# Kernel optimization log

Hardware: AMD Instinct MI355X
Metric: run time of the kernel (lower is better)

Reference implementation:

```python
import jax, jax.numpy as jnp
import numpy as np

D_MODEL = 1024
NUM_HEADS = 16
D_K = D_MODEL // NUM_HEADS
SCALE = float(np.sqrt(D_K))


def setup_inputs() -> dict:
    key = jax.random.key(0)
    ks = jax.random.split(key, 11)
    B, S = 2, 2048
    s = 0.02
    return {
        "query": jax.random.normal(ks[0], (B, S, D_MODEL), dtype=jnp.float32),
        "key_in": jax.random.normal(ks[1], (B, S, D_MODEL), dtype=jnp.float32),
        "value": jax.random.normal(ks[2], (B, S, D_MODEL), dtype=jnp.float32),
        "w_q": jax.random.normal(ks[3], (D_MODEL, D_MODEL), dtype=jnp.float32) * s,
        "b_q": jnp.zeros((D_MODEL,), dtype=jnp.float32),
        "w_k": jax.random.normal(ks[4], (D_MODEL, D_MODEL), dtype=jnp.float32) * s,
        "b_k": jnp.zeros((D_MODEL,), dtype=jnp.float32),
        "w_v": jax.random.normal(ks[5], (D_MODEL, D_MODEL), dtype=jnp.float32) * s,
        "b_v": jnp.zeros((D_MODEL,), dtype=jnp.float32),
        "w_o": jax.random.normal(ks[6], (D_MODEL, D_MODEL), dtype=jnp.float32) * s,
        "b_o": jnp.zeros((D_MODEL,), dtype=jnp.float32),
    }


def _mha(query, key_in, value, w_q, b_q, w_k, b_k, w_v, b_v, w_o, b_o):
    B, S, _ = query.shape
    # linear projections (x @ W + b), split into heads: [B, H, S, Dk]
    def proj(x, w, b):
        y = x @ w + b
        return y.reshape(B, -1, NUM_HEADS, D_K).transpose(0, 2, 1, 3)

    Q = proj(query, w_q, b_q)
    K = proj(key_in, w_k, b_k)
    V = proj(value, w_v, b_v)

    # scores: [B, H, Sq, Sk]
    scores = jnp.einsum("bhqd,bhkd->bhqk", Q, K) / SCALE
    attn = jax.nn.softmax(scores, axis=-1)  # dropout is identity in eval mode
    out = jnp.einsum("bhqk,bhkd->bhqd", attn, V)
    out = out.transpose(0, 2, 1, 3).reshape(B, S, D_MODEL)
    return out @ w_o + b_o


def reference(query, key_in, value, w_q, b_q, w_k, b_k, w_v, b_v, w_o, b_o):
    return _mha(query, key_in, value, w_q, b_q, w_k, b_k, w_v, b_v, w_o, b_o)
```

## Files before the change

### kernel.cpp

```cpp
#include <hip/hip_runtime.h>
#include <cstdint>

#define S_LEN 2048
#define DMODEL 1024
#define NHEADS 16
#define DK 64
#define BATCH 2
#define M_TOT 4096

typedef __attribute__((ext_vector_type(8)))  short  short8;
typedef __attribute__((ext_vector_type(4)))  float  f32x4;
typedef __attribute__((ext_vector_type(16))) float  f32x16;

__device__ __forceinline__ ushort f2bf(float f) {
    union { float f; uint32_t u; } v; v.f = f;
    uint32_t r = (v.u + 0x7fffu + ((v.u >> 16) & 1u)) >> 16;
    return (ushort)r;
}
__device__ __forceinline__ float bf2f(ushort u) {
    union { uint32_t u; float f; } v; v.u = ((uint32_t)u) << 16;
    return v.f;
}

__device__ __forceinline__ void gl_lds16(const void* g, void* l) {
    __builtin_amdgcn_global_load_lds(
        (const __attribute__((address_space(1))) void*)(g),
        (__attribute__((address_space(3))) void*)(l), 16, 0, 0);
}

__global__ __launch_bounds__(256)
void conv3_kernel(const float* __restrict__ a0, const float* __restrict__ a1,
                  const float* __restrict__ a2, ushort* __restrict__ o0,
                  ushort* __restrict__ o1, ushort* __restrict__ o2, int n8)
{
    const float*  in  = blockIdx.z == 0 ? a0 : (blockIdx.z == 1 ? a1 : a2);
    ushort*       out = blockIdx.z == 0 ? o0 : (blockIdx.z == 1 ? o1 : o2);
    int i = blockIdx.x * 256 + threadIdx.x;
    const int stride = gridDim.x * 256;
    for (; i < n8; i += stride) {
        const float4* p = (const float4*)(in + (size_t)i * 8);
        float4 a = p[0], b = p[1];
        ushort r[8];
        r[0]=f2bf(a.x); r[1]=f2bf(a.y); r[2]=f2bf(a.z); r[3]=f2bf(a.w);
        r[4]=f2bf(b.x); r[5]=f2bf(b.y); r[6]=f2bf(b.z); r[7]=f2bf(b.w);
        *(ushort4*)(out + (size_t)i * 8)     = *(ushort4*)&r[0];
        *(ushort4*)(out + (size_t)i * 8 + 4) = *(ushort4*)&r[4];
    }
}

__global__ __launch_bounds__(256)
void wtrans3_kernel(const float* __restrict__ wq, const float* __restrict__ wk,
                    const float* __restrict__ wv, ushort* __restrict__ oq,
                    ushort* __restrict__ ok, ushort* __restrict__ ov)
{
    const float* w  = blockIdx.z == 0 ? wq : (blockIdx.z == 1 ? wk : wv);
    ushort*      hi = blockIdx.z == 0 ? oq : (blockIdx.z == 1 ? ok : ov);

    __shared__ float t[64][65];
    const int n0 = blockIdx.x * 64, k0 = blockIdx.y * 64;
    const int r  = threadIdx.x >> 2;
    const int cb = (threadIdx.x & 3) * 16;

    #pragma unroll
    for (int j = 0; j < 4; ++j) {
        float4 v = *(const float4*)(w + (size_t)(k0 + r) * DMODEL + n0 + cb + j * 4);
        t[r][cb + j*4 + 0] = v.x;
        t[r][cb + j*4 + 1] = v.y;
        t[r][cb + j*4 + 2] = v.z;
        t[r][cb + j*4 + 3] = v.w;
    }
    __syncthreads();

    ushort h8[16];
    #pragma unroll
    for (int j = 0; j < 16; ++j) h8[j] = f2bf(t[cb + j][r]);
    ushort* dsth = hi + (size_t)(n0 + r) * DMODEL + k0 + cb;
    *(ushort4*)(dsth + 0)  = *(ushort4*)&h8[0];
    *(ushort4*)(dsth + 4)  = *(ushort4*)&h8[4];
    *(ushort4*)(dsth + 8)  = *(ushort4*)&h8[8];
    *(ushort4*)(dsth + 12) = *(ushort4*)&h8[12];
}

__global__ __launch_bounds__(256)
void wtrans_o_kernel(const float* __restrict__ w, ushort* __restrict__ hi,
                     ushort* __restrict__ lo)
{
    __shared__ float t[64][65];
    const int n0 = blockIdx.x * 64, k0 = blockIdx.y * 64;
    const int r  = threadIdx.x >> 2;
    const int cb = (threadIdx.x & 3) * 16;

    #pragma unroll
    for (int j = 0; j < 4; ++j) {
        float4 v = *(const float4*)(w + (size_t)(k0 + r) * DMODEL + n0 + cb + j * 4);
        t[r][cb + j*4 + 0] = v.x;
        t[r][cb + j*4 + 1] = v.y;
        t[r][cb + j*4 + 2] = v.z;
        t[r][cb + j*4 + 3] = v.w;
    }
    __syncthreads();

    ushort h8[16], l8[16];
    #pragma unroll
    for (int j = 0; j < 16; ++j) {
        float x = t[cb + j][r];
        ushort h = f2bf(x);
        h8[j] = h;
        l8[j] = f2bf(x - bf2f(h));
    }
    ushort* dsth = hi + (size_t)(n0 + r) * DMODEL + k0 + cb;
    ushort* dstl = lo + (size_t)(n0 + r) * DMODEL + k0 + cb;
    #pragma unroll
    for (int j = 0; j < 4; ++j) {
        *(ushort4*)(dsth + j*4) = *(ushort4*)&h8[j*4];
        *(ushort4*)(dstl + j*4) = *(ushort4*)&l8[j*4];
    }
}

template<int OMODE>
__global__ __launch_bounds__(256)
void gemm_bf16_kernel(const ushort* __restrict__ A, const ushort* __restrict__ Bt,
                      const float* __restrict__ bias, ushort* __restrict__ out,
                      float oscale)
{
    __shared__ __align__(16) ushort lds[2][12288];

    const int t = threadIdx.x, wv = t >> 6, lane = t & 63;
    const int c = lane & 15, g = lane >> 4;
    const int m0 = blockIdx.y * 128, n0 = blockIdx.x * 64;
    const int wr = wv >> 1, wc = wv & 1;
    const int lrow = lane >> 3, lcol = lane & 7;

    f32x4 acc[4][2];
    #pragma unroll
    for (int i = 0; i < 4; ++i)
        #pragma unroll
        for (int j = 0; j < 2; ++j)
            acc[i][j] = (f32x4){0.f, 0.f, 0.f, 0.f};

    auto stage = [&](int buf, int kt) {
        #pragma unroll
        for (int j = 0; j < 6; ++j) {
            const int ci = wv * 6 + j;
            ushort* dst = &lds[buf][ci * 512];
            const ushort* src;
            if (ci < 16) {
                const int row  = ci * 8 + lrow;
                const int colb = (lcol * 16) ^ ((row & 7) << 4);
                src = A + (size_t)(m0 + row) * 1024 + kt * 64 + (colb >> 1);
            } else {
                const int row  = (ci - 16) * 8 + lrow;
                const int colb = (lcol * 16) ^ ((row & 7) << 4);
                src = Bt + (size_t)(n0 + row) * 1024 + kt * 64 + (colb >> 1);
            }
            gl_lds16(src, dst);
        }
    };

    stage(0, 0);
    __syncthreads();

    for (int kt = 0; kt < 16; ++kt) {
        const int cur = kt & 1;
        if (kt < 15) stage(cur ^ 1, kt + 1);

        const char* la = (const char*)&lds[cur][0];
        const char* lb = (const char*)&lds[cur][8192];
        #pragma unroll
        for (int kk = 0; kk < 2; ++kk) {
            short8 af[4], bf[2];
            #pragma unroll
            for (int mf = 0; mf < 4; ++mf) {
                const int row = wr * 64 + mf * 16 + c;
                af[mf] = *(const short8*)(la + row * 128 +
                          ((kk * 64 + g * 16) ^ ((c & 7) << 4)));
            }
            #pragma unroll
            for (int nf = 0; nf < 2; ++nf) {
                const int row = wc * 32 + nf * 16 + c;
                bf[nf] = *(const short8*)(lb + row * 128 +
                          ((kk * 64 + g * 16) ^ ((c & 7) << 4)));
            }
            #pragma unroll
            for (int mf = 0; mf < 4; ++mf)
                #pragma unroll
                for (int nf = 0; nf < 2; ++nf)
                    acc[mf][nf] = __builtin_amdgcn_mfma_f32_16x16x32_bf16(
                        af[mf], bf[nf], acc[mf][nf], 0, 0, 0);
        }
        __syncthreads();
    }

    const int b      = m0 >> 11;
    const int s_base = m0 & 2047;
    #pragma unroll
    for (int nf = 0; nf < 2; ++nf) {
        const int ncol = n0 + wc * 32 + nf * 16 + c;
        const float bv = bias[ncol];
        const int h = ncol >> 6, dk = ncol & 63;
        #pragma unroll
        for (int mf = 0; mf < 4; ++mf) {
            if (OMODE == 1) {
                #pragma unroll
                for (int j = 0; j < 4; ++j) {
                    const int s = s_base + wr * 64 + mf * 16 + g * 4 + j;
                    out[(((size_t)(b * NHEADS + h) * S_LEN + s) * DK) + dk] =
                        f2bf((acc[mf][nf][j] + bv) * oscale);
                }
            } else {
                ushort4 v4;
                v4.x = f2bf((acc[mf][nf][0] + bv) * oscale);
                v4.y = f2bf((acc[mf][nf][1] + bv) * oscale);
                v4.z = f2bf((acc[mf][nf][2] + bv) * oscale);
                v4.w = f2bf((acc[mf][nf][3] + bv) * oscale);
                const int s = s_base + wr * 64 + mf * 16 + g * 4;
                *(ushort4*)&out[((size_t)(b * NHEADS + h) * DK + dk) * S_LEN + s] = v4;
            }
        }
    }
}

__global__ __launch_bounds__(256)
void gemm_split_kernel(const ushort* __restrict__ Ahi, const ushort* __restrict__ Alo,
                       const ushort* __restrict__ Bhi, const ushort* __restrict__ Blo,
                       const float* __restrict__ bias, float* __restrict__ out)
{
    __shared__ __align__(16) ushort lds[24576];

    const int t = threadIdx.x, wv = t >> 6, lane = t & 63;
    const int c = lane & 15, g = lane >> 4;
    const int m0 = blockIdx.y * 128, n0 = blockIdx.x * 64;
    const int wr = wv >> 1, wc = wv & 1;
    const int lrow = lane >> 3, lcol = lane & 7;

    f32x4 acc[4][2];
    #pragma unroll
    for (int i = 0; i < 4; ++i)
        #pragma unroll
        for (int j = 0; j < 2; ++j)
            acc[i][j] = (f32x4){0.f, 0.f, 0.f, 0.f};

    for (int kt = 0; kt < 16; ++kt) {
        if (kt) __syncthreads();
        #pragma unroll
        for (int j = 0; j < 12; ++j) {
            const int ci = wv * 12 + j;
            ushort* dst = &lds[ci * 512];
            const ushort* src;
            int row, colb;
            if (ci < 16) {
                row = ci * 8 + lrow; colb = (lcol*16) ^ ((row&7)<<4);
                src = Ahi + (size_t)(m0+row)*1024 + kt*64 + (colb>>1);
            } else if (ci < 32) {
                row = (ci-16)*8 + lrow; colb = (lcol*16) ^ ((row&7)<<4);
                src = Alo + (size_t)(m0+row)*1024 + kt*64 + (colb>>1);
            } else if (ci < 40) {
                row = (ci-32)*8 + lrow; colb = (lcol*16) ^ ((row&7)<<4);
                src = Bhi + (size_t)(n0+row)*1024 + kt*64 + (colb>>1);
            } else {
                row = (ci-40)*8 + lrow; colb = (lcol*16) ^ ((row&7)<<4);
                src = Blo + (size_t)(n0+row)*1024 + kt*64 + (colb>>1);
            }
            gl_lds16(src, dst);
        }
        __syncthreads();

        const char* lah = (const char*)&lds[0];
        const char* lal = (const char*)&lds[8192];
        const char* lbh = (const char*)&lds[16384];
        const char* lbl = (const char*)&lds[20480];
        #pragma unroll
        for (int kk = 0; kk < 2; ++kk) {
            short8 ah[4], al[4], bh[2], bl[2];
            #pragma unroll
            for (int mf = 0; mf < 4; ++mf) {
                const int row = wr*64 + mf*16 + c;
                const int off = row*128 + ((kk*64 + g*16) ^ ((c&7)<<4));
                ah[mf] = *(const short8*)(lah + off);
                al[mf] = *(const short8*)(lal + off);
            }
            #pragma unroll
            for (int nf = 0; nf < 2; ++nf) {
                const int row = wc*32 + nf*16 + c;
                const int off = row*128 + ((kk*64 + g*16) ^ ((c&7)<<4));
                bh[nf] = *(const short8*)(lbh + off);
                bl[nf] = *(const short8*)(lbl + off);
            }
            #pragma unroll
            for (int mf = 0; mf < 4; ++mf)
                #pragma unroll
                for (int nf = 0; nf < 2; ++nf) {
                    acc[mf][nf] = __builtin_amdgcn_mfma_f32_16x16x32_bf16(ah[mf], bh[nf], acc[mf][nf], 0,0,0);
                    acc[mf][nf] = __builtin_amdgcn_mfma_f32_16x16x32_bf16(ah[mf], bl[nf], acc[mf][nf], 0,0,0);
                    acc[mf][nf] = __builtin_amdgcn_mfma_f32_16x16x32_bf16(al[mf], bh[nf], acc[mf][nf], 0,0,0);
                }
        }
    }

    #pragma unroll
    for (int nf = 0; nf < 2; ++nf) {
        const int ncol = n0 + wc*32 + nf*16 + c;
        const float bv = bias[ncol];
        #pragma unroll
        for (int mf = 0; mf < 4; ++mf)
            #pragma unroll
            for (int j = 0; j < 4; ++j) {
                const int m = m0 + wr*64 + mf*16 + g*4 + j;
                out[(size_t)m * 1024 + ncol] = acc[mf][nf][j] + bv;
            }
    }
}

__global__ __launch_bounds__(256, 2)
void attn_kernel4(const ushort* __restrict__ Qh, const ushort* __restrict__ Kh,
                  const ushort* __restrict__ Vt, ushort* __restrict__ ctx_hi,
                  ushort* __restrict__ ctx_lo)
{
    __shared__ __align__(16) ushort KV[2][8192];

    const int t  = threadIdx.x, wv = t >> 6, lane = t & 63;
    const int q  = lane & 31;
    const int hi = lane >> 5;
    const int bh = blockIdx.y;
    const int q0 = blockIdx.x * 128 + wv * 32;

    const ushort* Kb = Kh + (size_t)bh * S_LEN * DK;
    const ushort* Vb = Vt + (size_t)bh * DK * S_LEN;
    const ushort* Qb = Qh + ((size_t)bh * S_LEN + q0 + q) * DK;

    short8 qf[4];
    #pragma unroll
    for (int s = 0; s < 4; ++s)
        qf[s] = *(const short8*)(Qb + s * 16 + hi * 8);

    const ushort* sbase[4];
    int sstr[4];
    char* dbase[4];
    #pragma unroll
    for (int j = 0; j < 4; ++j) {
        const int D = (j * 256 + t) * 16;
        dbase[j] = (char*)&KV[0][0] + D;
        if (D < 8192) {
            const int row = D >> 7;
            const int X   = D & 127;
            const int Xs  = X ^ ((row & 7) << 4);
            sbase[j] = Kb + row * DK + (Xs >> 1);
            sstr[j]  = DK;
        } else {
            const int Y   = D - 8192;
            const int kk  = Y >> 12;
            const int Z   = Y & 4095;
            const int r   = Z >> 7;
            const int gsl = ((Z & 127) >> 4) ^ (r & 7);
            const int d   = r + ((gsl >> 2) << 5);
            sbase[j] = Vb + (size_t)d * S_LEN + kk * 32 + (gsl & 3) * 8;
            sstr[j]  = 1;
        }
    }
    auto stage = [&](int buf, int k0) {
        #pragma unroll
        for (int j = 0; j < 4; ++j)
            gl_lds16(sbase[j] + (size_t)k0 * sstr[j], dbase[j] + buf * 16384);
    };

    float m = -3.0e38f, l = 0.f;
    f32x16 accO[2];
    #pragma unroll
    for (int i = 0; i < 16; ++i) { accO[0][i] = 0.f; accO[1][i] = 0.f; }

    const int swz = (q & 7) << 4;

    stage(0, 0);
    __syncthreads();

    for (int kt = 0; kt < 32; ++kt) {
        const int cur = kt & 1;
        if (kt < 31) stage(cur ^ 1, (kt + 1) * 64);

        const char* Kl = (const char*)&KV[cur][0];
        const char* Vl = Kl + 8192;

        #pragma unroll
        for (int kk = 0; kk < 2; ++kk) {
            f32x16 sa;
            #pragma unroll
            for (int i = 0; i < 16; ++i) sa[i] = 0.f;
            #pragma unroll
            for (int s = 0; s < 4; ++s) {
                short8 kf = *(const short8*)(Kl + (kk * 32 + q) * 128 +
                                             ((s * 32 + hi * 16) ^ swz));
                sa = __builtin_amdgcn_mfma_f32_32x32x16_bf16(kf, qf[s], sa, 0, 0, 0);
            }

            float mt = sa[0];
            #pragma unroll
            for (int r = 1; r < 16; ++r) mt = fmaxf(mt, sa[r]);
            mt = fmaxf(mt, __shfl_xor(mt, 32));

            if (__any(mt > m + 8.f)) {
                const float mnew = fmaxf(m, mt);
                const float corr = __builtin_amdgcn_exp2f(m - mnew);
                #pragma unroll
                for (int r = 0; r < 16; ++r) { accO[0][r] *= corr; accO[1][r] *= corr; }
                l *= corr;
                m = mnew;
            }

            float p[16], ps = 0.f;
            #pragma unroll
            for (int r = 0; r < 16; ++r) {
                p[r] = __builtin_amdgcn_exp2f(sa[r] - m);
                ps += p[r];
            }
            ps += __shfl_xor(ps, 32);
            l += ps;

            uint32_t u[8];
            #pragma unroll
            for (int jj = 0; jj < 8; ++jj)
                asm("v_cvt_pk_bf16_f32 %0, %1, %2"
                    : "=v"(u[jj]) : "v"(p[2*jj]), "v"(p[2*jj+1]));
            asm("v_permlane32_swap_b32 %0, %1" : "+v"(u[0]), "+v"(u[2]));
            asm("v_permlane32_swap_b32 %0, %1" : "+v"(u[1]), "+v"(u[3]));
            asm("v_permlane32_swap_b32 %0, %1" : "+v"(u[4]), "+v"(u[6]));
            asm("v_permlane32_swap_b32 %0, %1" : "+v"(u[5]), "+v"(u[7]));
            union { uint32_t w[4]; short8 s8; } pb0, pb1;
            pb0.w[0]=u[0]; pb0.w[1]=u[1]; pb0.w[2]=u[2]; pb0.w[3]=u[3];
            pb1.w[0]=u[4]; pb1.w[1]=u[5]; pb1.w[2]=u[6]; pb1.w[3]=u[7];

            const char* Vg = Vl + kk * 4096;
            #pragma unroll
            for (int db = 0; db < 2; ++db) {
                short8 vf0 = *(const short8*)(Vg + q * 128 + ((db*64 +      hi*16) ^ swz));
                short8 vf1 = *(const short8*)(Vg + q * 128 + ((db*64 + 32 + hi*16) ^ swz));
                accO[db] = __builtin_amdgcn_mfma_f32_32x32x16_bf16(vf0, pb0.s8, accO[db], 0, 0, 0);
                accO[db] = __builtin_amdgcn_mfma_f32_32x32x16_bf16(vf1, pb1.s8, accO[db], 0, 0, 0);
            }
        }
        __syncthreads();
    }

    const float inv = 1.f / l;
    const int b = bh >> 4, h = bh & 15;
    ushort* base_hi = ctx_hi + ((size_t)b * S_LEN + q0 + q) * DMODEL + h * DK;
    ushort* base_lo = ctx_lo + ((size_t)b * S_LEN + q0 + q) * DMODEL + h * DK;
    #pragma unroll
    for (int db = 0; db < 2; ++db)
        #pragma unroll
        for (int r = 0; r < 16; ++r) {
            const int d = db * 32 + (r & 3) + 8 * (r >> 2) + 4 * hi;
            const float val = accO[db][r] * inv;
            const ushort vh = f2bf(val);
            base_hi[d] = vh;
            base_lo[d] = f2bf(val - bf2f(vh));
        }
}

extern "C" void kernel_launch(void* const* d_in, const int* in_sizes, int n_in,
                              void* d_out, int out_size, void* d_ws, size_t ws_size,
                              hipStream_t stream)
{
    const float* query  = (const float*)d_in[0];
    const float* key_in = (const float*)d_in[1];
    const float* value  = (const float*)d_in[2];
    const float* w_q = (const float*)d_in[3];
    const float* b_q = (const float*)d_in[4];
    const float* w_k = (const float*)d_in[5];
    const float* b_k = (const float*)d_in[6];
    const float* w_v = (const float*)d_in[7];
    const float* b_v = (const float*)d_in[8];
    const float* w_o = (const float*)d_in[9];
    const float* b_o = (const float*)d_in[10];
    float* out = (float*)d_out;

    const size_t E4M = (size_t)M_TOT * DMODEL;
    const size_t E1M = (size_t)DMODEL * DMODEL;

    ushort* ws = (ushort*)d_ws;
    ushort* Aq    = ws;
    ushort* Ak    = Aq + E4M;
    ushort* Av    = Ak + E4M;
    ushort* Qh    = Av + E4M;
    ushort* Kh    = Qh + E4M;
    ushort* Vt    = Kh + E4M;
    ushort* Wq    = Vt + E4M;
    ushort* Wk    = Wq + E1M;
    ushort* Wv    = Wk + E1M;
    ushort* Wo_hi = Wv + E1M;
    ushort* Wo_lo = Wo_hi + E1M;
    ushort* ctx_hi = Aq;
    ushort* ctx_lo = Ak;

    const float qscale = 0.125f * 1.44269504088896340736f;

    dim3 blk(256);
    hipLaunchKernelGGL(conv3_kernel, dim3(512, 1, 3), blk, 0, stream,
                       query, key_in, value, Aq, Ak, Av, (int)(E4M / 8));
    hipLaunchKernelGGL(wtrans3_kernel, dim3(16, 16, 3), blk, 0, stream,
                       w_q, w_k, w_v, Wq, Wk, Wv);
    hipLaunchKernelGGL(wtrans_o_kernel, dim3(16, 16), blk, 0, stream,
                       w_o, Wo_hi, Wo_lo);

    dim3 ggrd(DMODEL / 64, M_TOT / 128);
    hipLaunchKernelGGL((gemm_bf16_kernel<1>), ggrd, blk, 0, stream, Aq, Wq, b_q, Qh, qscale);
    hipLaunchKernelGGL((gemm_bf16_kernel<1>), ggrd, blk, 0, stream, Ak, Wk, b_k, Kh, 1.0f);
    hipLaunchKernelGGL((gemm_bf16_kernel<2>), ggrd, blk, 0, stream, Av, Wv, b_v, Vt, 1.0f);

    dim3 agrd(S_LEN / 128, BATCH * NHEADS);
    hipLaunchKernelGGL(attn_kernel4, agrd, blk, 0, stream, Qh, Kh, Vt, ctx_hi, ctx_lo);

    hipLaunchKernelGGL(gemm_split_kernel, ggrd, blk, 0, stream,
                       ctx_hi, ctx_lo, Wo_hi, Wo_lo, b_o, out);
}
```

Before: 149.4 us.

## Merge QKV GEMMs and weight transposes, drop ctx lo split, double-buffer O-proj

Merges the three QKV projection GEMMs into one launch indexed by blockIdx.z, and merges the four weight-transpose kernels into one. The attention output is now written as a single bf16 tensor instead of a hi/lo pair, so the output projection does two MFMAs per fragment instead of three and gains a double-buffered LDS pipeline. Attention also gets an extra XOR term in the LDS swizzle and uses v_max3 for the row max. This cuts launch count, memory traffic and MFMA work, but lowers precision in the final projection and raises LDS use in the O GEMM.

```diff
diff --git a/kernel.cpp b/kernel.cpp
--- a/kernel.cpp
+++ b/kernel.cpp
@@ -20,6 +20,11 @@
 __device__ __forceinline__ float bf2f(ushort u) {
     union { uint32_t u; float f; } v; v.u = ((uint32_t)u) << 16;
     return v.f;
+}
+__device__ __forceinline__ float max3f(float a, float b, float c) {
+    float d;
+    asm("v_max3_f32 %0, %1, %2, %3" : "=v"(d) : "v"(a), "v"(b), "v"(c));
+    return d;
 }
 
 __device__ __forceinline__ void gl_lds16(const void* g, void* l) {
@@ -49,12 +54,16 @@
 }
 
 __global__ __launch_bounds__(256)
-void wtrans3_kernel(const float* __restrict__ wq, const float* __restrict__ wk,
-                    const float* __restrict__ wv, ushort* __restrict__ oq,
-                    ushort* __restrict__ ok, ushort* __restrict__ ov)
+void wtrans4_kernel(const float* __restrict__ wq, const float* __restrict__ wk,
+                    const float* __restrict__ wv, const float* __restrict__ wo,
+                    ushort* __restrict__ oq, ushort* __restrict__ ok,
+                    ushort* __restrict__ ov, ushort* __restrict__ oo_hi,
+                    ushort* __restrict__ oo_lo)
 {
-    const float* w  = blockIdx.z == 0 ? wq : (blockIdx.z == 1 ? wk : wv);
-    ushort*      hi = blockIdx.z == 0 ? oq : (blockIdx.z == 1 ? ok : ov);
+    const int z = blockIdx.z;
+    const float* w  = z == 0 ? wq : (z == 1 ? wk : (z == 2 ? wv : wo));
+    ushort*      hi = z == 0 ? oq : (z == 1 ? ok : (z == 2 ? ov : oo_hi));
+    const bool   LO = (z == 3);
 
     __shared__ float t[64][65];
     const int n0 = blockIdx.x * 64, k0 = blockIdx.y * 64;
@@ -71,35 +80,6 @@
     }
     __syncthreads();
 
-    ushort h8[16];
-    #pragma unroll
-    for (int j = 0; j < 16; ++j) h8[j] = f2bf(t[cb + j][r]);
-    ushort* dsth = hi + (size_t)(n0 + r) * DMODEL + k0 + cb;
-    *(ushort4*)(dsth + 0)  = *(ushort4*)&h8[0];
-    *(ushort4*)(dsth + 4)  = *(ushort4*)&h8[4];
-    *(ushort4*)(dsth + 8)  = *(ushort4*)&h8[8];
-    *(ushort4*)(dsth + 12) = *(ushort4*)&h8[12];
-}
-
-__global__ __launch_bounds__(256)
-void wtrans_o_kernel(const float* __restrict__ w, ushort* __restrict__ hi,
-                     ushort* __restrict__ lo)
-{
-    __shared__ float t[64][65];
-    const int n0 = blockIdx.x * 64, k0 = blockIdx.y * 64;
-    const int r  = threadIdx.x >> 2;
-    const int cb = (threadIdx.x & 3) * 16;
-
-    #pragma unroll
-    for (int j = 0; j < 4; ++j) {
-        float4 v = *(const float4*)(w + (size_t)(k0 + r) * DMODEL + n0 + cb + j * 4);
-        t[r][cb + j*4 + 0] = v.x;
-        t[r][cb + j*4 + 1] = v.y;
-        t[r][cb + j*4 + 2] = v.z;
-        t[r][cb + j*4 + 3] = v.w;
-    }
-    __syncthreads();
-
     ushort h8[16], l8[16];
     #pragma unroll
     for (int j = 0; j < 16; ++j) {
@@ -109,20 +89,33 @@
         l8[j] = f2bf(x - bf2f(h));
     }
     ushort* dsth = hi + (size_t)(n0 + r) * DMODEL + k0 + cb;
-    ushort* dstl = lo + (size_t)(n0 + r) * DMODEL + k0 + cb;
-    #pragma unroll
-    for (int j = 0; j < 4; ++j) {
+    #pragma unroll
+    for (int j = 0; j < 4; ++j)
         *(ushort4*)(dsth + j*4) = *(ushort4*)&h8[j*4];
-        *(ushort4*)(dstl + j*4) = *(ushort4*)&l8[j*4];
-    }
-}
-
-template<int OMODE>
+    if (LO) {
+        ushort* dstl = oo_lo + (size_t)(n0 + r) * DMODEL + k0 + cb;
+        #pragma unroll
+        for (int j = 0; j < 4; ++j)
+            *(ushort4*)(dstl + j*4) = *(ushort4*)&l8[j*4];
+    }
+}
+
 __global__ __launch_bounds__(256)
-void gemm_bf16_kernel(const ushort* __restrict__ A, const ushort* __restrict__ Bt,
-                      const float* __restrict__ bias, ushort* __restrict__ out,
-                      float oscale)
+void gemm_qkv_kernel(const ushort* __restrict__ Aq, const ushort* __restrict__ Ak,
+                     const ushort* __restrict__ Av, const ushort* __restrict__ Wq,
+                     const ushort* __restrict__ Wk, const ushort* __restrict__ Wv,
+                     const float* __restrict__ bq, const float* __restrict__ bk,
+                     const float* __restrict__ bv, ushort* __restrict__ Qh,
+                     ushort* __restrict__ Kh, ushort* __restrict__ Vt, float qscale)
 {
+    const int z = blockIdx.z;
+    const ushort* A    = z == 0 ? Aq : (z == 1 ? Ak : Av);
+    const ushort* Bt   = z == 0 ? Wq : (z == 1 ? Wk : Wv);
+    const float*  bias = z == 0 ? bq : (z == 1 ? bk : bv);
+    ushort*       out  = z == 0 ? Qh : (z == 1 ? Kh : Vt);
+    const float oscale = z == 0 ? qscale : 1.0f;
+    const int   mode   = z == 2 ? 2 : 1;
+
     __shared__ __align__(16) ushort lds[2][12288];
 
     const int t = threadIdx.x, wv = t >> 6, lane = t & 63;
@@ -200,7 +193,7 @@
         const int h = ncol >> 6, dk = ncol & 63;
         #pragma unroll
         for (int mf = 0; mf < 4; ++mf) {
-            if (OMODE == 1) {
+            if (mode == 1) {
                 #pragma unroll
                 for (int j = 0; j < 4; ++j) {
                     const int s = s_base + wr * 64 + mf * 16 + g * 4 + j;
@@ -209,10 +202,10 @@
                 }
             } else {
                 ushort4 v4;
-                v4.x = f2bf((acc[mf][nf][0] + bv) * oscale);
-                v4.y = f2bf((acc[mf][nf][1] + bv) * oscale);
-                v4.z = f2bf((acc[mf][nf][2] + bv) * oscale);
-                v4.w = f2bf((acc[mf][nf][3] + bv) * oscale);
+                v4.x = f2bf(acc[mf][nf][0] + bv);
+                v4.y = f2bf(acc[mf][nf][1] + bv);
+                v4.z = f2bf(acc[mf][nf][2] + bv);
+                v4.w = f2bf(acc[mf][nf][3] + bv);
                 const int s = s_base + wr * 64 + mf * 16 + g * 4;
                 *(ushort4*)&out[((size_t)(b * NHEADS + h) * DK + dk) * S_LEN + s] = v4;
             }
@@ -221,11 +214,11 @@
 }
 
 __global__ __launch_bounds__(256)
-void gemm_split_kernel(const ushort* __restrict__ Ahi, const ushort* __restrict__ Alo,
-                       const ushort* __restrict__ Bhi, const ushort* __restrict__ Blo,
-                       const float* __restrict__ bias, float* __restrict__ out)
+void gemm_o2_kernel(const ushort* __restrict__ A, const ushort* __restrict__ Bhi,
+                    const ushort* __restrict__ Blo, const float* __restrict__ bias,
+                    float* __restrict__ out)
 {
-    __shared__ __align__(16) ushort lds[24576];
+    __shared__ __align__(16) ushort lds[2][16384];
 
     const int t = threadIdx.x, wv = t >> 6, lane = t & 63;
     const int c = lane & 15, g = lane >> 4;
@@ -240,81 +233,83 @@
         for (int j = 0; j < 2; ++j)
             acc[i][j] = (f32x4){0.f, 0.f, 0.f, 0.f};
 
+    auto stage = [&](int buf, int kt) {
+        #pragma unroll
+        for (int j = 0; j < 8; ++j) {
+            const int ci = wv * 8 + j;
+            ushort* dst = &lds[buf][ci * 512];
+            const ushort* src;
+            if (ci < 16) {
+                const int row  = ci * 8 + lrow;
+                const int colb = (lcol * 16) ^ ((row & 7) << 4);
+                src = A + (size_t)(m0 + row) * 1024 + kt * 64 + (colb >> 1);
+            } else if (ci < 24) {
+                const int row  = (ci - 16) * 8 + lrow;
+                const int colb = (lcol * 16) ^ ((row & 7) << 4);
+                src = Bhi + (size_t)(n0 + row) * 1024 + kt * 64 + (colb >> 1);
+            } else {
+                const int row  = (ci - 24) * 8 + lrow;
+                const int colb = (lcol * 16) ^ ((row & 7) << 4);
+                src = Blo + (size_t)(n0 + row) * 1024 + kt * 64 + (colb >> 1);
+            }
+            gl_lds16(src, dst);
+        }
+    };
+
+    stage(0, 0);
+    __syncthreads();
+
     for (int kt = 0; kt < 16; ++kt) {
-        if (kt) __syncthreads();
-        #pragma unroll
-        for (int j = 0; j < 12; ++j) {
-            const int ci = wv * 12 + j;
-            ushort* dst = &lds[ci * 512];
-            const ushort* src;
-            int row, colb;
-            if (ci < 16) {
-                row = ci * 8 + lrow; colb = (lcol*16) ^ ((row&7)<<4);
-                src = Ahi + (size_t)(m0+row)*1024 + kt*64 + (colb>>1);
-            } else if (ci < 32) {
-                row = (ci-16)*8 + lrow; colb = (lcol*16) ^ ((row&7)<<4);
-                src = Alo + (size_t)(m0+row)*1024 + kt*64 + (colb>>1);
-            } else if (ci < 40) {
-                row = (ci-32)*8 + lrow; colb = (lcol*16) ^ ((row&7)<<4);
-                src = Bhi + (size_t)(n0+row)*1024 + kt*64 + (colb>>1);
-            } else {
-                row = (ci-40)*8 + lrow; colb = (lcol*16) ^ ((row&7)<<4);
-                src = Blo + (size_t)(n0+row)*1024 + kt*64 + (colb>>1);
-            }
-            gl_lds16(src, dst);
-        }
-        __syncthreads();
-
-        const char* lah = (const char*)&lds[0];
-        const char* lal = (const char*)&lds[8192];
-        const char* lbh = (const char*)&lds[16384];
-        const char* lbl = (const char*)&lds[20480];
+        const int cur = kt & 1;
+        if (kt < 15) stage(cur ^ 1, kt + 1);
+
+        const char* la = (const char*)&lds[cur][0];
+        const char* lh = (const char*)&lds[cur][8192];
+        const char* ll = (const char*)&lds[cur][12288];
         #pragma unroll
         for (int kk = 0; kk < 2; ++kk) {
-            short8 ah[4], al[4], bh[2], bl[2];
+            short8 af[4], bh[2], bl[2];
             #pragma unroll
             for (int mf = 0; mf < 4; ++mf) {
-                const int row = wr*64 + mf*16 + c;
-                const int off = row*128 + ((kk*64 + g*16) ^ ((c&7)<<4));
-                ah[mf] = *(const short8*)(lah + off);
-                al[mf] = *(const short8*)(lal + off);
+                const int row = wr * 64 + mf * 16 + c;
+                af[mf] = *(const short8*)(la + row * 128 +
+                          ((kk * 64 + g * 16) ^ ((c & 7) << 4)));
             }
             #pragma unroll
             for (int nf = 0; nf < 2; ++nf) {
-                const int row = wc*32 + nf*16 + c;
-                const int off = row*128 + ((kk*64 + g*16) ^ ((c&7)<<4));
-                bh[nf] = *(const short8*)(lbh + off);
-                bl[nf] = *(const short8*)(lbl + off);
+                const int row = wc * 32 + nf * 16 + c;
+                const int off = row * 128 + ((kk * 64 + g * 16) ^ ((c & 7) << 4));
+                bh[nf] = *(const short8*)(lh + off);
+                bl[nf] = *(const short8*)(ll + off);
             }
             #pragma unroll
             for (int mf = 0; mf < 4; ++mf)
                 #pragma unroll
                 for (int nf = 0; nf < 2; ++nf) {
-                    acc[mf][nf] = __builtin_amdgcn_mfma_f32_16x16x32_bf16(ah[mf], bh[nf], acc[mf][nf], 0,0,0);
-                    acc[mf][nf] = __builtin_amdgcn_mfma_f32_16x16x32_bf16(ah[mf], bl[nf], acc[mf][nf], 0,0,0);
-                    acc[mf][nf] = __builtin_amdgcn_mfma_f32_16x16x32_bf16(al[mf], bh[nf], acc[mf][nf], 0,0,0);
+                    acc[mf][nf] = __builtin_amdgcn_mfma_f32_16x16x32_bf16(af[mf], bh[nf], acc[mf][nf], 0,0,0);
+                    acc[mf][nf] = __builtin_amdgcn_mfma_f32_16x16x32_bf16(af[mf], bl[nf], acc[mf][nf], 0,0,0);
                 }
         }
+        __syncthreads();
     }
 
     #pragma unroll
     for (int nf = 0; nf < 2; ++nf) {
-        const int ncol = n0 + wc*32 + nf*16 + c;
+        const int ncol = n0 + wc * 32 + nf * 16 + c;
         const float bv = bias[ncol];
         #pragma unroll
         for (int mf = 0; mf < 4; ++mf)
             #pragma unroll
             for (int j = 0; j < 4; ++j) {
-                const int m = m0 + wr*64 + mf*16 + g*4 + j;
+                const int m = m0 + wr * 64 + mf * 16 + g * 4 + j;
                 out[(size_t)m * 1024 + ncol] = acc[mf][nf][j] + bv;
             }
     }
 }
 
 __global__ __launch_bounds__(256, 2)
-void attn_kernel4(const ushort* __restrict__ Qh, const ushort* __restrict__ Kh,
-                  const ushort* __restrict__ Vt, ushort* __restrict__ ctx_hi,
-                  ushort* __restrict__ ctx_lo)
+void attn_kernel5(const ushort* __restrict__ Qh, const ushort* __restrict__ Kh,
+                  const ushort* __restrict__ Vt, ushort* __restrict__ ctx)
 {
     __shared__ __align__(16) ushort KV[2][8192];
 
@@ -343,7 +338,7 @@
         if (D < 8192) {
             const int row = D >> 7;
             const int X   = D & 127;
-            const int Xs  = X ^ ((row & 7) << 4);
+            const int Xs  = X ^ ((((row & 7) ^ ((row >> 3) & 3))) << 4);
             sbase[j] = Kb + row * DK + (Xs >> 1);
             sstr[j]  = DK;
         } else {
@@ -351,7 +346,7 @@
             const int kk  = Y >> 12;
             const int Z   = Y & 4095;
             const int r   = Z >> 7;
-            const int gsl = ((Z & 127) >> 4) ^ (r & 7);
+            const int gsl = ((Z & 127) >> 4) ^ ((r & 7) ^ ((r >> 3) & 3));
             const int d   = r + ((gsl >> 2) << 5);
             sbase[j] = Vb + (size_t)d * S_LEN + kk * 32 + (gsl & 3) * 8;
             sstr[j]  = 1;
@@ -368,7 +363,7 @@
     #pragma unroll
     for (int i = 0; i < 16; ++i) { accO[0][i] = 0.f; accO[1][i] = 0.f; }
 
-    const int swz = (q & 7) << 4;
+    const int swz = ((q & 7) ^ ((q >> 3) & 3)) << 4;
 
     stage(0, 0);
     __syncthreads();
@@ -392,9 +387,12 @@
                 sa = __builtin_amdgcn_mfma_f32_32x32x16_bf16(kf, qf[s], sa, 0, 0, 0);
             }
 
-            float mt = sa[0];
-            #pragma unroll
-            for (int r = 1; r < 16; ++r) mt = fmaxf(mt, sa[r]);
+            float m0_ = max3f(sa[0],  sa[1],  sa[2]);
+            float m1_ = max3f(sa[3],  sa[4],  sa[5]);
+            float m2_ = max3f(sa[6],  sa[7],  sa[8]);
+            float m3_ = max3f(sa[9],  sa[10], sa[11]);
+            float m4_ = max3f(sa[12], sa[13], sa[14]);
+            float mt  = fmaxf(max3f(m0_, m1_, m2_), max3f(m3_, m4_, sa[15]));
             mt = fmaxf(mt, __shfl_xor(mt, 32));
 
             if (__any(mt > m + 8.f)) {
@@ -442,17 +440,13 @@
 
     const float inv = 1.f / l;
     const int b = bh >> 4, h = bh & 15;
-    ushort* base_hi = ctx_hi + ((size_t)b * S_LEN + q0 + q) * DMODEL + h * DK;
-    ushort* base_lo = ctx_lo + ((size_t)b * S_LEN + q0 + q) * DMODEL + h * DK;
+    ushort* base = ctx + ((size_t)b * S_LEN + q0 + q) * DMODEL + h * DK;
     #pragma unroll
     for (int db = 0; db < 2; ++db)
         #pragma unroll
         for (int r = 0; r < 16; ++r) {
             const int d = db * 32 + (r & 3) + 8 * (r >> 2) + 4 * hi;
-            const float val = accO[db][r] * inv;
-            const ushort vh = f2bf(val);
-            base_hi[d] = vh;
-            base_lo[d] = f2bf(val - bf2f(vh));
+            base[d] = f2bf(accO[db][r] * inv);
         }
 }
 
@@ -488,27 +482,24 @@
     ushort* Wv    = Wk + E1M;
     ushort* Wo_hi = Wv + E1M;
     ushort* Wo_lo = Wo_hi + E1M;
-    ushort* ctx_hi = Aq;
-    ushort* ctx_lo = Ak;
+    ushort* ctx   = Aq;
 
     const float qscale = 0.125f * 1.44269504088896340736f;
 
     dim3 blk(256);
     hipLaunchKernelGGL(conv3_kernel, dim3(512, 1, 3), blk, 0, stream,
                        query, key_in, value, Aq, Ak, Av, (int)(E4M / 8));
-    hipLaunchKernelGGL(wtrans3_kernel, dim3(16, 16, 3), blk, 0, stream,
-                       w_q, w_k, w_v, Wq, Wk, Wv);
-    hipLaunchKernelGGL(wtrans_o_kernel, dim3(16, 16), blk, 0, stream,
-                       w_o, Wo_hi, Wo_lo);
-
-    dim3 ggrd(DMODEL / 64, M_TOT / 128);
-    hipLaunchKernelGGL((gemm_bf16_kernel<1>), ggrd, blk, 0, stream, Aq, Wq, b_q, Qh, qscale);
-    hipLaunchKernelGGL((gemm_bf16_kernel<1>), ggrd, blk, 0, stream, Ak, Wk, b_k, Kh, 1.0f);
-    hipLaunchKernelGGL((gemm_bf16_kernel<2>), ggrd, blk, 0, stream, Av, Wv, b_v, Vt, 1.0f);
+    hipLaunchKernelGGL(wtrans4_kernel, dim3(16, 16, 4), blk, 0, stream,
+                       w_q, w_k, w_v, w_o, Wq, Wk, Wv, Wo_hi, Wo_lo);
+
+    dim3 ggrd(DMODEL / 64, M_TOT / 128, 3);
+    hipLaunchKernelGGL(gemm_qkv_kernel, ggrd, blk, 0, stream,
+                       Aq, Ak, Av, Wq, Wk, Wv, b_q, b_k, b_v, Qh, Kh, Vt, qscale);
 
     dim3 agrd(S_LEN / 128, BATCH * NHEADS);
-    hipLaunchKernelGGL(attn_kernel4, agrd, blk, 0, stream, Qh, Kh, Vt, ctx_hi, ctx_lo);
-
-    hipLaunchKernelGGL(gemm_split_kernel, ggrd, blk, 0, stream,
-                       ctx_hi, ctx_lo, Wo_hi, Wo_lo, b_o, out);
-}
+    hipLaunchKernelGGL(attn_kernel5, agrd, blk, 0, stream, Qh, Kh, Vt, ctx);
+
+    dim3 ogrd(DMODEL / 64, M_TOT / 128);
+    hipLaunchKernelGGL(gemm_o2_kernel, ogrd, blk, 0, stream,
+                       ctx, Wo_hi, Wo_lo, b_o, out);
+}
```

Result: faster. 130.3 us (-12.8%).
